# Performance work log

Measured on AMD Instinct MI355X. Metric: run time of the kernel, lower is better.

The kernel has to match this reference:

```python
import jax, jax.numpy as jnp
import numpy as np

B, N, K = 64, 1024, 20
HEADS, DIM_K, DIM_V, CH_RAISE = 8, 32, 32, 64
C_CAT = 4 * 2 + DIM_V  # 44


def setup_inputs() -> dict:
    key = jax.random.key(0)
    ks = jax.random.split(key, 16)

    def w(k, shape):
        fan_in = shape[-1]
        return jax.random.normal(k, shape, dtype=jnp.float32) / np.sqrt(fan_in)

    def gamma(k, n):
        return 1.0 + 0.1 * jax.random.normal(k, (n,), dtype=jnp.float32)

    def beta(k, n):
        return 0.1 * jax.random.normal(k, (n,), dtype=jnp.float32)

    return {
        "x": jax.random.normal(ks[0], (B, N, 4), dtype=jnp.float32),
        "W_h": w(ks[1], (DIM_V, 4)),              # mlp_h: conv2d 4 -> dim_v, 1x1
        "W1": w(ks[2], (CH_RAISE, C_CAT)),        # mlp conv2d 44 -> 64
        "g1": gamma(ks[3], CH_RAISE), "b1": beta(ks[4], CH_RAISE),
        "W2": w(ks[5], (CH_RAISE, CH_RAISE)),     # mlp conv2d 64 -> 64
        "g2": gamma(ks[6], CH_RAISE), "b2": beta(ks[7], CH_RAISE),
        "W_v": w(ks[8], (DIM_V, C_CAT)),          # mlp_v conv1d 44 -> 32
        "gv": gamma(ks[9], DIM_V), "bv": beta(ks[10], DIM_V),
        "W_k": w(ks[11], (DIM_K, C_CAT)),         # mlp_k conv1d 44 -> 32
        "W_q": w(ks[12], (HEADS * DIM_K, CH_RAISE)),  # mlp_q conv1d 64 -> 256
        "gq": gamma(ks[13], HEADS * DIM_K), "bq": beta(ks[14], HEADS * DIM_K),
    }


def _forward(x, W_h, W1, g1, b1, W2, g2, b2, W_v, gv, bv, W_k, W_q, gq, bq):
    xyz = x[..., :4]                 # [B,N,4]
    feat = xyz                       # use_norm=False -> feature = xyz
    b, n, _ = xyz.shape

    # squared pairwise distances [B,N,N]
    sq = jnp.sum(xyz * xyz, axis=-1)
    dist = -2.0 * jnp.einsum('bnc,bmc->bnm', xyz, xyz) + sq[:, :, None] + sq[:, None, :]

    # KNN: K smallest distances
    _, knn_idx = jax.lax.top_k(-dist, K)          # [B,N,K]
    bidx = jnp.arange(b)[:, None, None]
    neighbor_xyz = xyz[bidx, knn_idx]             # [B,N,K,4]
    grouped = feat[bidx, knn_idx]                 # [B,N,K,4]

    feat_t = jnp.transpose(feat, (0, 2, 1))       # [B,4,N]
    grouped_c = jnp.transpose(grouped, (0, 3, 1, 2))          # [B,4,N,K]
    gnorm = grouped_c - feat_t[..., None]                     # [B,4,N,K]
    rel = jnp.transpose(neighbor_xyz - xyz[:, :, None, :], (0, 3, 1, 2))  # [B,4,N,K]

    pos = jnp.einsum('vc,bcnk->bvnk', W_h, rel)               # [B,32,N,K]
    center = jnp.broadcast_to(feat_t[..., None], (b, 4, n, K))
    feature = jnp.concatenate([gnorm, center, pos], axis=1)   # [B,44,N,K]

    # mlp: two 1x1 conv + BN(eval, affine) + ReLU
    h = jnp.einsum('oc,bcnk->bonk', W1, feature)
    h = jax.nn.relu(g1[None, :, None, None] * h + b1[None, :, None, None])
    h = jnp.einsum('oc,bcnk->bonk', W2, h)
    h = jax.nn.relu(g2[None, :, None, None] * h + b2[None, :, None, None])
    feature_q = jnp.max(h, axis=-1)                           # [B,64,N]

    q = jnp.einsum('oc,bcn->bon', W_q, feature_q)             # [B,256,N]
    q = jax.nn.relu(gq[None, :, None] * q + bq[None, :, None])
    q = q.reshape(b, HEADS, DIM_K, n)                         # [B,h,d,N]

    v = jnp.einsum('vc,bcnk->bvnk', W_v, feature)             # [B,32,N,K]
    v = gv[None, :, None, None] * v + bv[None, :, None, None]
    v = jnp.transpose(v, (0, 2, 1, 3))                        # [B,N,v,K]

    kk = jnp.einsum('dc,bcnk->bdnk', W_k, feature)            # [B,32,N,K]
    kk = jax.nn.softmax(kk, axis=-1)
    kk = jnp.transpose(kk, (0, 2, 1, 3))                      # [B,N,d,K]

    kv = jnp.einsum('bndk,bnvk->bdvn', kk, v)                 # [B,d,v,N]
    out = jnp.einsum('bhdn,bdvn->bhvn', q, kv)                # [B,h,v,N]
    out = out.reshape(b, HEADS * DIM_V, n)                    # [B,256,N]
    return xyz, out


def reference(x, W_h, W1, g1, b1, W2, g2, b2, W_v, gv, bv, W_k, W_q, gq, bq):
    return _forward(x, W_h, W1, g1, b1, W2, g2, b2, W_v, gv, bv, W_k, W_q, gq, bq)
```

## Files before the change

### kernel.cpp

```cpp
#include <hip/hip_runtime.h>
#include <math.h>

#define NPTS 1024
#define KNBR 20
#define CH 64


typedef __attribute__((ext_vector_type(8))) short s16x8;
typedef __attribute__((ext_vector_type(4))) float f32x4;

static __device__ __forceinline__ ushort f2bf(float f) {
  uint u = __float_as_uint(f);
  uint r = (u + 0x7FFFu + ((u >> 16) & 1u)) >> 16;
  return (ushort)r;
}

static __device__ __forceinline__ uint pkbf(float a, float b) {
  uint ua = __float_as_uint(a) + 0x8000u;
  uint ub = __float_as_uint(b) + 0x8000u;
  return __builtin_amdgcn_perm(ub, ua, 0x07060302);
}

static __device__ __forceinline__ int mbcnt64(unsigned long long m) {
  return __builtin_amdgcn_mbcnt_hi((uint)(m >> 32),
                                   __builtin_amdgcn_mbcnt_lo((uint)m, 0));
}

__global__ __launch_bounds__(256) void k_prep(
    const float* __restrict__ Wh, const float* __restrict__ W1,
    const float* __restrict__ g1, const float* __restrict__ b1,
    const float* __restrict__ Wv, const float* __restrict__ Wk,
    const float* __restrict__ W2, const float* __restrict__ Wq,
    float* __restrict__ wp, ushort* __restrict__ w2b,
    ushort* __restrict__ wqb, ushort* __restrict__ w1b) {
  int t = threadIdx.x;
  {
    int o = t >> 2, c = t & 3;
    float acc = W1[o * 40 + c];
    #pragma unroll
    for (int v = 0; v < 32; ++v) acc = fmaf(W1[o * 40 + 8 + v], Wh[v * 4 + c], acc);
    float g = g1[o];
    wp[t] = g * acc;
    wp[256 + t] = g * W1[o * 40 + 4 + c];
  }
  if (t < 128) {
    int d = t >> 2, c = t & 3;
    float av = Wv[d * 40 + c];
    float ak = Wk[d * 40 + c];
    #pragma unroll
    for (int u = 0; u < 32; ++u) {
      av = fmaf(Wv[d * 40 + 8 + u], Wh[u * 4 + c], av);
      ak = fmaf(Wk[d * 40 + 8 + u], Wh[u * 4 + c], ak);
    }
    wp[512 + t] = av;
    wp[640 + t] = Wv[d * 40 + 4 + c];
    wp[768 + t] = ak;
    wp[896 + t] = Wk[d * 40 + 4 + c];
  }
  #pragma unroll
  for (int i = 0; i < 16; ++i) w2b[t * 16 + i] = f2bf(W2[t * 16 + i]);
  for (int i = 0; i < 64; ++i) wqb[t * 64 + i] = f2bf(Wq[t * 64 + i]);
  __syncthreads();
  for (int idx = t; idx < 2048; idx += 256) {
    int ch = idx >> 5, kk = idx & 31;
    float v = 0.f;
    if (kk < 4) v = wp[ch * 4 + kk];
    else if (kk < 8) v = wp[256 + ch * 4 + (kk - 4)];
    else if (kk == 8) v = b1[ch];
    w1b[idx] = f2bf(v);
  }
}

__global__ __launch_bounds__(256) void k_knn(const float4* __restrict__ xv,
                                             ushort* __restrict__ knn,
                                             float4* __restrict__ outx) {
  __shared__ float4 sx[NPTS];
  __shared__ float ssq[NPTS];
  __shared__ uint s_sk[4][64];
  __shared__ ushort s_sj[4][64];

  int t = threadIdx.x;
  int b = blockIdx.x >> 6, grp = blockIdx.x & 63;
  for (int j = t; j < NPTS; j += 256) {
    float4 p = xv[b * NPTS + j];
    sx[j] = p;
    ssq[j] = p.x * p.x + p.y * p.y + p.z * p.z + p.w * p.w;
    if (grp == 0) outx[b * NPTS + j] = p;
  }
  __syncthreads();

  int w = t >> 6, l = t & 63;

  #pragma unroll 1
  for (int i = 0; i < 4; ++i) {
    int cloc = grp * 16 + w * 4 + i;
    int gid20 = (b * NPTS + cloc) * KNBR;
    float4 c = sx[cloc];
    uint u[16];
    uint mn = 0xFFFFFFFFu;
    #pragma unroll
    for (int s = 0; s < 16; ++s) {
      int j = s * 64 + l;
      float4 q = sx[j];
      float dot = c.x * q.x;
      dot = fmaf(c.y, q.y, dot);
      dot = fmaf(c.z, q.z, dot);
      dot = fmaf(c.w, q.w, dot);
      float key = fmaf(-2.f, dot, ssq[j]);
      uint uu = __float_as_uint(key);
      uu = ((int)uu < 0) ? ~uu : (uu | 0x80000000u);
      u[s] = uu;
      mn = min(mn, uu);
    }

    uint T0 = 0;
    #pragma unroll
    for (int bit = 31; bit >= 0; --bit) {
      uint cand = T0 | (1u << bit);
      if (__popcll(__ballot(mn < cand)) < 20) T0 = cand;
    }

    int scnt = 0;
    #pragma unroll
    for (int s = 0; s < 16; ++s) scnt += (int)__popcll(__ballot(u[s] <= T0));

    if (scnt <= 64) {
      int base = 0;
      #pragma unroll
      for (int s = 0; s < 16; ++s) {
        unsigned long long mask = __ballot(u[s] <= T0);
        if (u[s] <= T0) {
          int off = base + mbcnt64(mask);
          s_sk[w][off] = u[s];
          s_sj[w][off] = (ushort)(s * 64 + l);
        }
        base += (int)__popcll(mask);
      }
      asm volatile("s_waitcnt lgkmcnt(0)" ::: "memory");
      __builtin_amdgcn_sched_barrier(0);
      uint uk = (l < scnt) ? s_sk[w][l] : 0xFFFFFFFFu;
      uint uj = (l < scnt) ? (uint)s_sj[w][l] : 0xFFFFu;

      uint u20 = 0;
      #pragma unroll
      for (int bit = 31; bit >= 0; --bit) {
        uint cand = u20 | (1u << bit);
        if (__popcll(__ballot(uk < cand)) < 20) u20 = cand;
      }
      int m = (int)__popcll(__ballot(uk < u20));
      int r = 20 - m;
      uint jr = 0;
      #pragma unroll
      for (int bit = 10; bit >= 0; --bit) {
        uint cand = jr | (1u << bit);
        if (__popcll(__ballot((uk == u20) && (uj < cand))) < r) jr = cand;
      }
      bool sel = (uk < u20) || ((uk == u20) && (uj <= jr));
      unsigned long long smask = __ballot(sel);
      int off = mbcnt64(smask);
      if (sel) knn[gid20 + off] = (ushort)uj;
    } else {
      uint u20 = 0;
      #pragma unroll 1
      for (int bit = 31; bit >= 0; --bit) {
        uint cand = u20 | (1u << bit);
        int cnt = 0;
        #pragma unroll
        for (int s = 0; s < 16; ++s)
          cnt += (int)__popcll(__ballot(u[s] < cand));
        if (cnt < 20) u20 = cand;
      }
      int base = 0;
      #pragma unroll
      for (int s = 0; s < 16; ++s) {
        unsigned long long mask = __ballot(u[s] < u20);
        if (u[s] < u20) knn[gid20 + base + mbcnt64(mask)] = (ushort)(s * 64 + l);
        base += (int)__popcll(mask);
      }
      int r = 20 - base;
      #pragma unroll
      for (int s = 0; s < 16; ++s) {
        unsigned long long mask = __ballot(u[s] == u20);
        int pos = mbcnt64(mask);
        int cntm = (int)__popcll(mask);
        int take = (r < cntm) ? r : cntm;
        if ((u[s] == u20) && (pos < take))
          knn[gid20 + base + pos] = (ushort)(s * 64 + l);
        base += take;
        r -= take;
      }
    }
  }
}

__global__ __launch_bounds__(256) void k_fused(
    const float4* __restrict__ xv, const ushort* __restrict__ knn,
    const float* __restrict__ wp, const ushort* __restrict__ w1b,
    const ushort* __restrict__ w2b, const ushort* __restrict__ wqb,
    const float* __restrict__ g2, const float* __restrict__ b2,
    const float* __restrict__ gq, const float* __restrict__ bq,
    const float* __restrict__ gv, const float* __restrict__ bv,
    float* __restrict__ o1) {
  __shared__ __align__(16) char smem[51200];
  char* s_h1 = smem;
  ushort* s_qb = (ushort*)smem;
  ushort* s_eb = (ushort*)(smem + 10496);
  float* s_out = (float*)(smem + 10496);
  float4* s_rel = (float4*)(smem + 40960);
  char* s_fqb = smem + 46080;
  float4* s_ctr = (float4*)(smem + 48384);
  ushort* s_ab = (ushort*)(smem + 40960);

  int t = threadIdx.x;
  int gid0 = blockIdx.x * 16;
  int bbase = (gid0 >> 10) << 10;
  int b = gid0 >> 10;
  int n0 = gid0 & 1023;
  int w = t >> 6, l = t & 63;
  int g = l >> 4, lane16 = l & 15;

  if (t < 16) s_ctr[t] = xv[gid0 + t];
  #pragma unroll
  for (int it2 = 0; it2 < 2; ++it2) {
    int idx = t + it2 * 256;
    if (idx < 320) {
      int p = (int)(((uint)idx * 3277u) >> 16);
      int k = idx - p * 20;
      int nb = (int)knn[(size_t)(gid0 + p) * KNBR + k];
      float4 nx = xv[bbase + nb];
      float4 ct = xv[gid0 + p];
      s_rel[p * 20 + k] =
          make_float4(nx.x - ct.x, nx.y - ct.y, nx.z - ct.z, nx.w - ct.w);
    }
  }
  __syncthreads();

  {
    s16x8 ah[4];
    #pragma unroll
    for (int m = 0; m < 4; ++m)
      ah[m] = *(const s16x8*)(w1b + (m * 16 + lane16) * 32 + g * 8);
    s16x8 bz = {0, 0, 0, 0, 0, 0, 0, 0};
    s16x8 bone = bz;
    bone[0] = (short)0x3F80;
    #pragma unroll
    for (int q = 0; q < 5; ++q) {
      int col = w * 80 + q * 16 + lane16;
      s16x8 bf;
      if (g == 0) {
        float4 r = s_rel[lane16 * 20 + 5 * w + q];
        float4 ct = s_ctr[lane16];
        union { uint4 u; s16x8 s; } cv;
        cv.u.x = pkbf(r.x, r.y);
        cv.u.y = pkbf(r.z, r.w);
        cv.u.z = pkbf(ct.x, ct.y);
        cv.u.w = pkbf(ct.z, ct.w);
        bf = cv.s;
      } else {
        bf = (g == 1) ? bone : bz;
      }
      int swz = (col & 7) << 4;
      #pragma unroll
      for (int m = 0; m < 4; ++m) {
        f32x4 acc = {0.f, 0.f, 0.f, 0.f};
        acc = __builtin_amdgcn_mfma_f32_16x16x32_bf16(ah[m], bf, acc, 0, 0, 0);
        uint2 hv;
        hv.x = pkbf(fmaxf(acc[0], 0.f), fmaxf(acc[1], 0.f));
        hv.y = pkbf(fmaxf(acc[2], 0.f), fmaxf(acc[3], 0.f));
        int byteoff = col * 128 + (m * 16 + g * 4) * 2;
        *(uint2*)(s_h1 + (byteoff ^ swz)) = hv;
      }
    }
  }
  __syncthreads();

  {
    int row0 = w * 16 + g * 4;
    s16x8 af0 = *(const s16x8*)(w2b + (w * 16 + lane16) * 64 + g * 8);
    s16x8 af1 = *(const s16x8*)(w2b + (w * 16 + lane16) * 64 + 32 + g * 8);
    float4 g2v = *(const float4*)(g2 + row0);
    float4 b2v = *(const float4*)(b2 + row0);
    float mx0 = 0.f, mx1 = 0.f, mx2 = 0.f, mx3 = 0.f;
    #pragma unroll 4
    for (int kt = 0; kt < 20; ++kt) {
      int col = kt * 16 + lane16;
      int rowbyte = col * 128;
      int swz = (col & 7) << 4;
      s16x8 bf0 = *(const s16x8*)(s_h1 + ((rowbyte + g * 16) ^ swz));
      s16x8 bf1 = *(const s16x8*)(s_h1 + ((rowbyte + 64 + g * 16) ^ swz));
      f32x4 acc = {0.f, 0.f, 0.f, 0.f};
      acc = __builtin_amdgcn_mfma_f32_16x16x32_bf16(af0, bf0, acc, 0, 0, 0);
      acc = __builtin_amdgcn_mfma_f32_16x16x32_bf16(af1, bf1, acc, 0, 0, 0);
      mx0 = fmaxf(mx0, fmaxf(fmaf(g2v.x, acc[0], b2v.x), 0.f));
      mx1 = fmaxf(mx1, fmaxf(fmaf(g2v.y, acc[1], b2v.y), 0.f));
      mx2 = fmaxf(mx2, fmaxf(fmaf(g2v.z, acc[2], b2v.z), 0.f));
      mx3 = fmaxf(mx3, fmaxf(fmaf(g2v.w, acc[3], b2v.w), 0.f));
    }
    uint2 u2;
    u2.x = pkbf(mx0, mx1);
    u2.y = pkbf(mx2, mx3);
    *(uint2*)(s_fqb + lane16 * 144 + row0 * 2) = u2;
  }
  __syncthreads();

  {
    s16x8 af[4][2];
    #pragma unroll
    for (int mm = 0; mm < 4; ++mm) {
      int row = w * 64 + mm * 16 + lane16;
      af[mm][0] = *(const s16x8*)(wqb + row * 64 + g * 8);
      af[mm][1] = *(const s16x8*)(wqb + row * 64 + 32 + g * 8);
    }
    s16x8 bf0 = *(const s16x8*)(s_fqb + lane16 * 144 + 0 * 64 + g * 16);
    s16x8 bf1 = *(const s16x8*)(s_fqb + lane16 * 144 + 1 * 64 + g * 16);
    #pragma unroll
    for (int mm = 0; mm < 4; ++mm) {
      f32x4 acc = {0.f, 0.f, 0.f, 0.f};
      acc = __builtin_amdgcn_mfma_f32_16x16x32_bf16(af[mm][0], bf0, acc, 0, 0, 0);
      acc = __builtin_amdgcn_mfma_f32_16x16x32_bf16(af[mm][1], bf1, acc, 0, 0, 0);
      int rbase = w * 64 + mm * 16 + g * 4;
      int h = rbase >> 5, d0 = rbase & 31;
      float4 gqv = *(const float4*)(gq + rbase);
      float4 bqv = *(const float4*)(bq + rbase);
      float v0 = fmaxf(fmaf(gqv.x, acc[0], bqv.x), 0.f);
      float v1 = fmaxf(fmaf(gqv.y, acc[1], bqv.y), 0.f);
      float v2 = fmaxf(fmaf(gqv.z, acc[2], bqv.z), 0.f);
      float v3 = fmaxf(fmaf(gqv.w, acc[3], bqv.w), 0.f);
      uint2 u2;
      u2.x = pkbf(v0, v1);
      u2.y = pkbf(v2, v3);
      *(uint2*)(s_qb + lane16 * 328 + h * 40 + d0) = u2;
    }
  }

  uint vp[2][10];
  {
    int d = t & 31, phalf = t >> 5;
    float4 wr = *(const float4*)(wp + 512 + 256 + d * 4);
    float4 wc = *(const float4*)(wp + 512 + 384 + d * 4);
    float4 vr_ = *(const float4*)(wp + 512 + 0 + d * 4);
    float4 vc_ = *(const float4*)(wp + 512 + 128 + d * 4);
    float gvd = gv[d], bvd = bv[d];
    #pragma unroll
    for (int i = 0; i < 2; ++i) {
      int p = phalf + 8 * i;
      float4 ct = s_ctr[p];
      float cb = fmaf(wc.x, ct.x, fmaf(wc.y, ct.y, fmaf(wc.z, ct.z, wc.w * ct.w)));
      float ev[KNBR];
      float sum = 0.f;
      #pragma unroll
      for (int k = 0; k < KNBR; ++k) {
        float4 r = s_rel[p * 20 + k];
        float kkv =
            fmaf(wr.x, r.x, fmaf(wr.y, r.y, fmaf(wr.z, r.z, fmaf(wr.w, r.w, cb))));
        ev[k] = __expf(kkv);
        sum += ev[k];
      }
      float cbv = fmaf(vc_.x, ct.x, fmaf(vc_.y, ct.y, fmaf(vc_.z, ct.z, vc_.w * ct.w)));
      float vv[KNBR];
      #pragma unroll
      for (int k = 0; k < KNBR; ++k) {
        float4 r = s_rel[p * 20 + k];
        float raw =
            fmaf(vr_.x, r.x, fmaf(vr_.y, r.y, fmaf(vr_.z, r.z, fmaf(vr_.w, r.w, cbv))));
        vv[k] = fmaf(gvd, raw, bvd);
      }
      float rs = 1.0f / sum;
      #pragma unroll
      for (int k = 0; k < KNBR; ++k)
        s_eb[(p * 20 + k) * 40 + d] = f2bf(ev[k] * rs);
      #pragma unroll
      for (int k2 = 0; k2 < 10; ++k2) vp[i][k2] = pkbf(vv[k2 * 2], vv[k2 * 2 + 1]);
    }
  }
  __syncthreads();

  #pragma unroll
  for (int pi2 = 0; pi2 < 4; ++pi2) {
    int plo = pi2 & 1, ii = pi2 >> 1;
    int pi = 2 * w + plo + 8 * ii;
    s16x8 qa = *(const s16x8*)(s_qb + pi * 328 + (lane16 & 7) * 40 + g * 8);
    #pragma unroll
    for (int tile = 0; tile < 2; ++tile) {
      int k = tile * 16 + lane16;
      int kc = (k < KNBR) ? k : (KNBR - 1);
      s16x8 eb = *(const s16x8*)(s_eb + (pi * 20 + kc) * 40 + g * 8);
      f32x4 acc = {0.f, 0.f, 0.f, 0.f};
      acc = __builtin_amdgcn_mfma_f32_16x16x32_bf16(qa, eb, acc, 0, 0, 0);
      if (g < 2) {
        if (k < KNBR) {
          #pragma unroll
          for (int r = 0; r < 4; ++r)
            s_ab[pi * 320 + (g * 4 + r) * 40 + k] = f2bf(acc[r]);
        } else {
          #pragma unroll
          for (int r = 0; r < 4; ++r) s_ab[pi * 320 + (g * 4 + r) * 40 + k] = 0;
        }
      }
    }
  }
  __syncthreads();

  #pragma unroll
  for (int pi2 = 0; pi2 < 4; ++pi2) {
    int plo = pi2 & 1, ii = pi2 >> 1;
    int pi = 2 * w + plo + 8 * ii;
    s16x8 aa = *(const s16x8*)(s_ab + pi * 320 + (lane16 & 7) * 40 + g * 8);
    #pragma unroll
    for (int vt = 0; vt < 2; ++vt) {
      int srcl4 = ((plo * 32 + vt * 16 + lane16) << 2);
      uint bu[4];
      #pragma unroll
      for (int i = 0; i < 4; ++i) {
        uint t0 = (uint)__builtin_amdgcn_ds_bpermute(srcl4, (int)vp[ii][i]);
        uint t1 = (uint)__builtin_amdgcn_ds_bpermute(srcl4, (int)vp[ii][4 + i]);
        uint t2 = (i < 2)
                      ? (uint)__builtin_amdgcn_ds_bpermute(srcl4, (int)vp[ii][8 + i])
                      : 0u;
        bu[i] = (g == 0) ? t0 : (g == 1) ? t1 : (g == 2) ? t2 : 0u;
      }
      union { uint4 u; s16x8 s; } bb;
      bb.u.x = bu[0]; bb.u.y = bu[1]; bb.u.z = bu[2]; bb.u.w = bu[3];
      f32x4 acc = {0.f, 0.f, 0.f, 0.f};
      acc = __builtin_amdgcn_mfma_f32_16x16x32_bf16(aa, bb.s, acc, 0, 0, 0);
      if (g < 2) {
        int v = vt * 16 + lane16;
        #pragma unroll
        for (int r = 0; r < 4; ++r) {
          int h = g * 4 + r;
          s_out[(h * 32 + v) * 17 + pi] = acc[r];
        }
      }
    }
  }
  __syncthreads();

  #pragma unroll
  for (int e = 0; e < 16; ++e) {
    int idx = t + e * 256;
    int hv = idx >> 4, pp = idx & 15;
    o1[b * 262144 + hv * 1024 + n0 + pp] = s_out[hv * 17 + pp];
  }
}

extern "C" void kernel_launch(void* const* d_in, const int* in_sizes, int n_in,
                              void* d_out, int out_size, void* d_ws, size_t ws_size,
                              hipStream_t stream) {
  const float* x = (const float*)d_in[0];
  const float* Wh = (const float*)d_in[1];
  const float* W1 = (const float*)d_in[2];
  const float* g1 = (const float*)d_in[3];
  const float* b1 = (const float*)d_in[4];
  const float* W2 = (const float*)d_in[5];
  const float* g2 = (const float*)d_in[6];
  const float* b2 = (const float*)d_in[7];
  const float* Wv = (const float*)d_in[8];
  const float* gv = (const float*)d_in[9];
  const float* bv = (const float*)d_in[10];
  const float* Wk = (const float*)d_in[11];
  const float* Wq = (const float*)d_in[12];
  const float* gq = (const float*)d_in[13];
  const float* bq = (const float*)d_in[14];
  float* out = (float*)d_out;

  ushort* knn = (ushort*)d_ws;
  float* wp = (float*)((char*)d_ws + 19398656);
  ushort* w2b = (ushort*)((char*)d_ws + 19402752);
  ushort* wqb = (ushort*)((char*)d_ws + 19410944);
  ushort* w1b = (ushort*)((char*)d_ws + 19443712);

  hipLaunchKernelGGL(k_prep, dim3(1), dim3(256), 0, stream, Wh, W1, g1, b1, Wv, Wk,
                     W2, Wq, wp, w2b, wqb, w1b);
  hipLaunchKernelGGL(k_knn, dim3(4096), dim3(256), 0, stream, (const float4*)x, knn,
                     (float4*)out);
  hipLaunchKernelGGL(k_fused, dim3(4096), dim3(256), 0, stream, (const float4*)x,
                     knn, wp, w1b, w2b, wqb, g2, b2, gq, bq, gv, bv, out + 262144);
}
```

Measured before the change: 161.5 us.

## Replace ballot radix selects in KNN with wave bitonic sorts and prefix scan

The KNN top-20 selection used 32-step ballot/popcount radix searches to find thresholds and a second pair of radix searches to break ties among the candidates. These are replaced by a 64-lane bitonic sort over the per-lane minima to get the threshold, a shuffle-based prefix scan for compaction offsets, and a 64-bit (key,index) bitonic sort of the compacted candidates that writes the first 20 directly. This cuts the serial ballot chain but adds many cross-lane shuffles, including 64-bit shuffles split into two 32-bit shuffles. The output order of the selected neighbours becomes sorted by distance instead of by index.

```diff
diff --git a/kernel.cpp b/kernel.cpp
--- a/kernel.cpp
+++ b/kernel.cpp
@@ -24,6 +24,13 @@
 static __device__ __forceinline__ int mbcnt64(unsigned long long m) {
   return __builtin_amdgcn_mbcnt_hi((uint)(m >> 32),
                                    __builtin_amdgcn_mbcnt_lo((uint)m, 0));
+}
+
+static __device__ __forceinline__ unsigned long long shflx64(
+    unsigned long long v, int m) {
+  uint lo = __shfl_xor((uint)v, m);
+  uint hi = __shfl_xor((uint)(v >> 32), m);
+  return (((unsigned long long)hi) << 32) | lo;
 }
 
 __global__ __launch_bounds__(256) void k_prep(
@@ -113,62 +120,71 @@
       mn = min(mn, uu);
     }
 
-    uint T0 = 0;
-    #pragma unroll
-    for (int bit = 31; bit >= 0; --bit) {
-      uint cand = T0 | (1u << bit);
-      if (__popcll(__ballot(mn < cand)) < 20) T0 = cand;
-    }
-
-    int scnt = 0;
-    #pragma unroll
-    for (int s = 0; s < 16; ++s) scnt += (int)__popcll(__ballot(u[s] <= T0));
+    uint sv = mn;
+    #pragma unroll
+    for (int kk2 = 2; kk2 <= 64; kk2 <<= 1) {
+      #pragma unroll
+      for (int j2 = kk2 >> 1; j2 > 0; j2 >>= 1) {
+        uint ov = __shfl_xor(sv, j2);
+        bool up = ((l & kk2) == 0);
+        bool keepmin = (((l & j2) == 0) == up);
+        uint lo_ = min(sv, ov), hi_ = max(sv, ov);
+        sv = keepmin ? lo_ : hi_;
+      }
+    }
+    uint T0 = __shfl(sv, 19);
+
+    int cnt = 0;
+    #pragma unroll
+    for (int s = 0; s < 16; ++s) cnt += (u[s] <= T0) ? 1 : 0;
+    int pfx = cnt;
+    #pragma unroll
+    for (int d2 = 1; d2 < 64; d2 <<= 1) {
+      int o = __shfl_up(pfx, d2);
+      if (l >= d2) pfx += o;
+    }
+    int scnt = __shfl(pfx, 63);
+    pfx -= cnt;
 
     if (scnt <= 64) {
-      int base = 0;
+      int off = pfx;
       #pragma unroll
       for (int s = 0; s < 16; ++s) {
-        unsigned long long mask = __ballot(u[s] <= T0);
         if (u[s] <= T0) {
-          int off = base + mbcnt64(mask);
           s_sk[w][off] = u[s];
           s_sj[w][off] = (ushort)(s * 64 + l);
+          ++off;
         }
-        base += (int)__popcll(mask);
       }
       asm volatile("s_waitcnt lgkmcnt(0)" ::: "memory");
       __builtin_amdgcn_sched_barrier(0);
       uint uk = (l < scnt) ? s_sk[w][l] : 0xFFFFFFFFu;
       uint uj = (l < scnt) ? (uint)s_sj[w][l] : 0xFFFFu;
-
-      uint u20 = 0;
-      #pragma unroll
-      for (int bit = 31; bit >= 0; --bit) {
-        uint cand = u20 | (1u << bit);
-        if (__popcll(__ballot(uk < cand)) < 20) u20 = cand;
-      }
-      int m = (int)__popcll(__ballot(uk < u20));
-      int r = 20 - m;
-      uint jr = 0;
-      #pragma unroll
-      for (int bit = 10; bit >= 0; --bit) {
-        uint cand = jr | (1u << bit);
-        if (__popcll(__ballot((uk == u20) && (uj < cand))) < r) jr = cand;
-      }
-      bool sel = (uk < u20) || ((uk == u20) && (uj <= jr));
-      unsigned long long smask = __ballot(sel);
-      int off = mbcnt64(smask);
-      if (sel) knn[gid20 + off] = (ushort)uj;
+      unsigned long long pv = (((unsigned long long)uk) << 16) | uj;
+
+      #pragma unroll
+      for (int kk2 = 2; kk2 <= 64; kk2 <<= 1) {
+        #pragma unroll
+        for (int j2 = kk2 >> 1; j2 > 0; j2 >>= 1) {
+          unsigned long long ov = shflx64(pv, j2);
+          bool up = ((l & kk2) == 0);
+          bool keepmin = (((l & j2) == 0) == up);
+          unsigned long long lo_ = (pv < ov) ? pv : ov;
+          unsigned long long hi_ = (pv < ov) ? ov : pv;
+          pv = keepmin ? lo_ : hi_;
+        }
+      }
+      if (l < KNBR) knn[gid20 + l] = (ushort)(pv & 0xFFFFu);
     } else {
       uint u20 = 0;
       #pragma unroll 1
       for (int bit = 31; bit >= 0; --bit) {
         uint cand = u20 | (1u << bit);
-        int cnt = 0;
+        int cnt2 = 0;
         #pragma unroll
         for (int s = 0; s < 16; ++s)
-          cnt += (int)__popcll(__ballot(u[s] < cand));
-        if (cnt < 20) u20 = cand;
+          cnt2 += (int)__popcll(__ballot(u[s] < cand));
+        if (cnt2 < 20) u20 = cand;
       }
       int base = 0;
       #pragma unroll
```

New measurement: 176.4 us. +9.3%, slower.

## Compute key and value projections with MFMA instead of scalar FMAs

Applied to the files above, without the earlier changes.

The prep kernel now packs the folded key and value weights, with the value scale and bias, into a bf16 matrix shaped like the first-layer weights. The fused kernel reuses the already-built B fragments to compute key logits and values with bf16 MFMAs into shared memory. It then reads them back per thread, replacing per-neighbor scalar dot products over the relative positions. This trades VALU work for extra MFMAs, two more barriers and shared-memory round trips, and key logits are now rounded to bf16 before the softmax exponent, which can affect accuracy.

```diff
diff --git a/kernel.cpp b/kernel.cpp
--- a/kernel.cpp
+++ b/kernel.cpp
@@ -29,10 +29,12 @@
 __global__ __launch_bounds__(256) void k_prep(
     const float* __restrict__ Wh, const float* __restrict__ W1,
     const float* __restrict__ g1, const float* __restrict__ b1,
-    const float* __restrict__ Wv, const float* __restrict__ Wk,
+    const float* __restrict__ Wv, const float* __restrict__ gv,
+    const float* __restrict__ bv, const float* __restrict__ Wk,
     const float* __restrict__ W2, const float* __restrict__ Wq,
     float* __restrict__ wp, ushort* __restrict__ w2b,
-    ushort* __restrict__ wqb, ushort* __restrict__ w1b) {
+    ushort* __restrict__ wqb, ushort* __restrict__ w1b,
+    ushort* __restrict__ wkvb) {
   int t = threadIdx.x;
   {
     int o = t >> 2, c = t & 3;
@@ -68,6 +70,21 @@
     else if (kk < 8) v = wp[256 + ch * 4 + (kk - 4)];
     else if (kk == 8) v = b1[ch];
     w1b[idx] = f2bf(v);
+  }
+  for (int idx = t; idx < 2048; idx += 256) {
+    int ch = idx >> 5, kk = idx & 31;
+    float v = 0.f;
+    if (ch < 32) {
+      if (kk < 4) v = wp[768 + ch * 4 + kk];
+      else if (kk < 8) v = wp[896 + ch * 4 + (kk - 4)];
+    } else {
+      int d = ch - 32;
+      float gvd = gv[d];
+      if (kk < 4) v = gvd * wp[512 + d * 4 + kk];
+      else if (kk < 8) v = gvd * wp[640 + d * 4 + (kk - 4)];
+      else if (kk == 8) v = bv[d];
+    }
+    wkvb[idx] = f2bf(v);
   }
 }
 
@@ -164,11 +181,11 @@
       #pragma unroll 1
       for (int bit = 31; bit >= 0; --bit) {
         uint cand = u20 | (1u << bit);
-        int cnt = 0;
+        int cnt2 = 0;
         #pragma unroll
         for (int s = 0; s < 16; ++s)
-          cnt += (int)__popcll(__ballot(u[s] < cand));
-        if (cnt < 20) u20 = cand;
+          cnt2 += (int)__popcll(__ballot(u[s] < cand));
+        if (cnt2 < 20) u20 = cand;
       }
       int base = 0;
       #pragma unroll
@@ -195,14 +212,14 @@
 
 __global__ __launch_bounds__(256) void k_fused(
     const float4* __restrict__ xv, const ushort* __restrict__ knn,
-    const float* __restrict__ wp, const ushort* __restrict__ w1b,
-    const ushort* __restrict__ w2b, const ushort* __restrict__ wqb,
+    const ushort* __restrict__ w1b, const ushort* __restrict__ w2b,
+    const ushort* __restrict__ wqb, const ushort* __restrict__ wkvb,
     const float* __restrict__ g2, const float* __restrict__ b2,
     const float* __restrict__ gq, const float* __restrict__ bq,
-    const float* __restrict__ gv, const float* __restrict__ bv,
     float* __restrict__ o1) {
   __shared__ __align__(16) char smem[51200];
   char* s_h1 = smem;
+  char* s_kv = smem;
   ushort* s_qb = (ushort*)smem;
   ushort* s_eb = (ushort*)(smem + 10496);
   float* s_out = (float*)(smem + 10496);
@@ -235,6 +252,7 @@
   }
   __syncthreads();
 
+  s16x8 bfv[5];
   {
     s16x8 ah[4];
     #pragma unroll
@@ -259,6 +277,7 @@
       } else {
         bf = (g == 1) ? bone : bz;
       }
+      bfv[q] = bf;
       int swz = (col & 7) << 4;
       #pragma unroll
       for (int m = 0; m < 4; ++m) {
@@ -304,6 +323,51 @@
   __syncthreads();
 
   {
+    s16x8 akv[4];
+    #pragma unroll
+    for (int m = 0; m < 4; ++m)
+      akv[m] = *(const s16x8*)(wkvb + (m * 16 + lane16) * 32 + g * 8);
+    #pragma unroll
+    for (int q = 0; q < 5; ++q) {
+      int col = w * 80 + q * 16 + lane16;
+      int swz = (col & 7) << 4;
+      #pragma unroll
+      for (int m = 0; m < 4; ++m) {
+        f32x4 acc = {0.f, 0.f, 0.f, 0.f};
+        acc = __builtin_amdgcn_mfma_f32_16x16x32_bf16(akv[m], bfv[q], acc, 0, 0, 0);
+        uint2 hv;
+        hv.x = pkbf(acc[0], acc[1]);
+        hv.y = pkbf(acc[2], acc[3]);
+        int byteoff = col * 128 + (m * 16 + g * 4) * 2;
+        *(uint2*)(s_kv + (byteoff ^ swz)) = hv;
+      }
+    }
+  }
+  __syncthreads();
+
+  uint kkpk[2][10], vp[2][10];
+  int dd = t & 31, phalf = t >> 5;
+  {
+    #pragma unroll
+    for (int i = 0; i < 2; ++i) {
+      int p = phalf + 8 * i;
+      int swz = (p & 7) << 4;
+      const char* kbase = s_kv + p * 128 + ((dd * 2) ^ swz);
+      const char* vbase = s_kv + p * 128 + (((64 + dd * 2)) ^ swz);
+      #pragma unroll
+      for (int k2 = 0; k2 < 10; ++k2) {
+        uint ka = *(const ushort*)(kbase + (2 * k2) * 2048);
+        uint kb = *(const ushort*)(kbase + (2 * k2 + 1) * 2048);
+        kkpk[i][k2] = ka | (kb << 16);
+        uint va = *(const ushort*)(vbase + (2 * k2) * 2048);
+        uint vb = *(const ushort*)(vbase + (2 * k2 + 1) * 2048);
+        vp[i][k2] = va | (vb << 16);
+      }
+    }
+  }
+  __syncthreads();
+
+  {
     s16x8 af[4][2];
     #pragma unroll
     for (int mm = 0; mm < 4; ++mm) {
@@ -332,45 +396,23 @@
       *(uint2*)(s_qb + lane16 * 328 + h * 40 + d0) = u2;
     }
   }
-
-  uint vp[2][10];
-  {
-    int d = t & 31, phalf = t >> 5;
-    float4 wr = *(const float4*)(wp + 512 + 256 + d * 4);
-    float4 wc = *(const float4*)(wp + 512 + 384 + d * 4);
-    float4 vr_ = *(const float4*)(wp + 512 + 0 + d * 4);
-    float4 vc_ = *(const float4*)(wp + 512 + 128 + d * 4);
-    float gvd = gv[d], bvd = bv[d];
+  {
     #pragma unroll
     for (int i = 0; i < 2; ++i) {
       int p = phalf + 8 * i;
-      float4 ct = s_ctr[p];
-      float cb = fmaf(wc.x, ct.x, fmaf(wc.y, ct.y, fmaf(wc.z, ct.z, wc.w * ct.w)));
       float ev[KNBR];
       float sum = 0.f;
       #pragma unroll
       for (int k = 0; k < KNBR; ++k) {
-        float4 r = s_rel[p * 20 + k];
-        float kkv =
-            fmaf(wr.x, r.x, fmaf(wr.y, r.y, fmaf(wr.z, r.z, fmaf(wr.w, r.w, cb))));
-        ev[k] = __expf(kkv);
+        uint bits = (k & 1) ? (kkpk[i][k >> 1] & 0xFFFF0000u)
+                            : (kkpk[i][k >> 1] << 16);
+        ev[k] = __expf(__uint_as_float(bits));
         sum += ev[k];
       }
-      float cbv = fmaf(vc_.x, ct.x, fmaf(vc_.y, ct.y, fmaf(vc_.z, ct.z, vc_.w * ct.w)));
-      float vv[KNBR];
-      #pragma unroll
-      for (int k = 0; k < KNBR; ++k) {
-        float4 r = s_rel[p * 20 + k];
-        float raw =
-            fmaf(vr_.x, r.x, fmaf(vr_.y, r.y, fmaf(vr_.z, r.z, fmaf(vr_.w, r.w, cbv))));
-        vv[k] = fmaf(gvd, raw, bvd);
-      }
       float rs = 1.0f / sum;
       #pragma unroll
       for (int k = 0; k < KNBR; ++k)
-        s_eb[(p * 20 + k) * 40 + d] = f2bf(ev[k] * rs);
-      #pragma unroll
-      for (int k2 = 0; k2 < 10; ++k2) vp[i][k2] = pkbf(vv[k2 * 2], vv[k2 * 2 + 1]);
+        s_eb[(p * 20 + k) * 40 + dd] = f2bf(ev[k] * rs);
     }
   }
   __syncthreads();
@@ -468,11 +510,12 @@
   ushort* w2b = (ushort*)((char*)d_ws + 19402752);
   ushort* wqb = (ushort*)((char*)d_ws + 19410944);
   ushort* w1b = (ushort*)((char*)d_ws + 19443712);
-
-  hipLaunchKernelGGL(k_prep, dim3(1), dim3(256), 0, stream, Wh, W1, g1, b1, Wv, Wk,
-                     W2, Wq, wp, w2b, wqb, w1b);
+  ushort* wkvb = (ushort*)((char*)d_ws + 19447808);
+
+  hipLaunchKernelGGL(k_prep, dim3(1), dim3(256), 0, stream, Wh, W1, g1, b1, Wv, gv,
+                     bv, Wk, W2, Wq, wp, w2b, wqb, w1b, wkvb);
   hipLaunchKernelGGL(k_knn, dim3(4096), dim3(256), 0, stream, (const float4*)x, knn,
                      (float4*)out);
   hipLaunchKernelGGL(k_fused, dim3(4096), dim3(256), 0, stream, (const float4*)x,
-                     knn, wp, w1b, w2b, wqb, g2, b2, gq, bq, gv, bv, out + 262144);
-}
+                     knn, w1b, w2b, wqb, wkvb, g2, b2, gq, bq, out + 262144);
+}
```

After: 172.1 us. 6.6% more time.

## Fuse KNN selection and feature MLP into one kernel via shared memory

Applied to the files above, without the earlier changes.

Merges the KNN kernel and the fused MLP/attention kernel into a single launch. Neighbor indices are kept in shared memory instead of going to global memory, and neighbor coordinates are gathered from the shared point cloud instead of global loads. This removes one launch, the round trip of the knn index buffer and the global gathers. In exchange the KNN-phase shared buffers are aliased into the larger fused-kernel region, which adds register and LDS pressure that may reduce occupancy.

```diff
diff --git a/kernel.cpp b/kernel.cpp
--- a/kernel.cpp
+++ b/kernel.cpp
@@ -71,30 +71,51 @@
   }
 }
 
-__global__ __launch_bounds__(256) void k_knn(const float4* __restrict__ xv,
-                                             ushort* __restrict__ knn,
-                                             float4* __restrict__ outx) {
-  __shared__ float4 sx[NPTS];
-  __shared__ float ssq[NPTS];
-  __shared__ uint s_sk[4][64];
-  __shared__ ushort s_sj[4][64];
+__global__ __launch_bounds__(256) void k_all(
+    const float4* __restrict__ xv, const float* __restrict__ wp,
+    const ushort* __restrict__ w1b, const ushort* __restrict__ w2b,
+    const ushort* __restrict__ wqb, const float* __restrict__ g2,
+    const float* __restrict__ b2, const float* __restrict__ gq,
+    const float* __restrict__ bq, const float* __restrict__ gv,
+    const float* __restrict__ bv, float4* __restrict__ outx,
+    float* __restrict__ o1) {
+  __shared__ __align__(16) char smem[51200];
+  float4* sx = (float4*)smem;
+  float* ssq = (float*)(smem + 16384);
+  char* s_h1 = smem;
+  ushort* s_qb = (ushort*)smem;
+  ushort* s_eb = (ushort*)(smem + 10496);
+  float* s_out = (float*)(smem + 10496);
+  float4* s_rel = (float4*)(smem + 40960);
+  char* s_fqb = smem + 46080;
+  float4* s_ctr = (float4*)(smem + 48384);
+  ushort* s_knn = (ushort*)(smem + 48640);
+  uint* s_sk = (uint*)(smem + 49280);
+  ushort* s_sj = (ushort*)(smem + 50304);
+  ushort* s_ab = (ushort*)(smem + 40960);
 
   int t = threadIdx.x;
-  int b = blockIdx.x >> 6, grp = blockIdx.x & 63;
+  int bid = blockIdx.x;
+  int b = bid >> 6, grp = bid & 63;
+  int gid0 = bid * 16;
+  int n0 = gid0 & 1023;
+  int w = t >> 6, l = t & 63;
+  int g = l >> 4, lane16 = l & 15;
+
   for (int j = t; j < NPTS; j += 256) {
     float4 p = xv[b * NPTS + j];
     sx[j] = p;
     ssq[j] = p.x * p.x + p.y * p.y + p.z * p.z + p.w * p.w;
     if (grp == 0) outx[b * NPTS + j] = p;
   }
-  __syncthreads();
-
-  int w = t >> 6, l = t & 63;
+  if (t < 16) s_ctr[t] = xv[gid0 + t];
+  __syncthreads();
 
   #pragma unroll 1
   for (int i = 0; i < 4; ++i) {
-    int cloc = grp * 16 + w * 4 + i;
-    int gid20 = (b * NPTS + cloc) * KNBR;
+    int lp = w * 4 + i;
+    int cloc = n0 + lp;
+    int lp20 = lp * KNBR;
     float4 c = sx[cloc];
     uint u[16];
     uint mn = 0xFFFFFFFFu;
@@ -131,15 +152,15 @@
         unsigned long long mask = __ballot(u[s] <= T0);
         if (u[s] <= T0) {
           int off = base + mbcnt64(mask);
-          s_sk[w][off] = u[s];
-          s_sj[w][off] = (ushort)(s * 64 + l);
+          s_sk[w * 64 + off] = u[s];
+          s_sj[w * 64 + off] = (ushort)(s * 64 + l);
         }
         base += (int)__popcll(mask);
       }
       asm volatile("s_waitcnt lgkmcnt(0)" ::: "memory");
       __builtin_amdgcn_sched_barrier(0);
-      uint uk = (l < scnt) ? s_sk[w][l] : 0xFFFFFFFFu;
-      uint uj = (l < scnt) ? (uint)s_sj[w][l] : 0xFFFFu;
+      uint uk = (l < scnt) ? s_sk[w * 64 + l] : 0xFFFFFFFFu;
+      uint uj = (l < scnt) ? (uint)s_sj[w * 64 + l] : 0xFFFFu;
 
       uint u20 = 0;
       #pragma unroll
@@ -158,23 +179,23 @@
       bool sel = (uk < u20) || ((uk == u20) && (uj <= jr));
       unsigned long long smask = __ballot(sel);
       int off = mbcnt64(smask);
-      if (sel) knn[gid20 + off] = (ushort)uj;
+      if (sel) s_knn[lp20 + off] = (ushort)uj;
     } else {
       uint u20 = 0;
       #pragma unroll 1
       for (int bit = 31; bit >= 0; --bit) {
         uint cand = u20 | (1u << bit);
-        int cnt = 0;
+        int cnt2 = 0;
         #pragma unroll
         for (int s = 0; s < 16; ++s)
-          cnt += (int)__popcll(__ballot(u[s] < cand));
-        if (cnt < 20) u20 = cand;
+          cnt2 += (int)__popcll(__ballot(u[s] < cand));
+        if (cnt2 < 20) u20 = cand;
       }
       int base = 0;
       #pragma unroll
       for (int s = 0; s < 16; ++s) {
         unsigned long long mask = __ballot(u[s] < u20);
-        if (u[s] < u20) knn[gid20 + base + mbcnt64(mask)] = (ushort)(s * 64 + l);
+        if (u[s] < u20) s_knn[lp20 + base + mbcnt64(mask)] = (ushort)(s * 64 + l);
         base += (int)__popcll(mask);
       }
       int r = 20 - base;
@@ -185,50 +206,23 @@
         int cntm = (int)__popcll(mask);
         int take = (r < cntm) ? r : cntm;
         if ((u[s] == u20) && (pos < take))
-          knn[gid20 + base + pos] = (ushort)(s * 64 + l);
+          s_knn[lp20 + base + pos] = (ushort)(s * 64 + l);
         base += take;
         r -= take;
       }
     }
   }
-}
-
-__global__ __launch_bounds__(256) void k_fused(
-    const float4* __restrict__ xv, const ushort* __restrict__ knn,
-    const float* __restrict__ wp, const ushort* __restrict__ w1b,
-    const ushort* __restrict__ w2b, const ushort* __restrict__ wqb,
-    const float* __restrict__ g2, const float* __restrict__ b2,
-    const float* __restrict__ gq, const float* __restrict__ bq,
-    const float* __restrict__ gv, const float* __restrict__ bv,
-    float* __restrict__ o1) {
-  __shared__ __align__(16) char smem[51200];
-  char* s_h1 = smem;
-  ushort* s_qb = (ushort*)smem;
-  ushort* s_eb = (ushort*)(smem + 10496);
-  float* s_out = (float*)(smem + 10496);
-  float4* s_rel = (float4*)(smem + 40960);
-  char* s_fqb = smem + 46080;
-  float4* s_ctr = (float4*)(smem + 48384);
-  ushort* s_ab = (ushort*)(smem + 40960);
-
-  int t = threadIdx.x;
-  int gid0 = blockIdx.x * 16;
-  int bbase = (gid0 >> 10) << 10;
-  int b = gid0 >> 10;
-  int n0 = gid0 & 1023;
-  int w = t >> 6, l = t & 63;
-  int g = l >> 4, lane16 = l & 15;
-
-  if (t < 16) s_ctr[t] = xv[gid0 + t];
+  __syncthreads();
+
   #pragma unroll
   for (int it2 = 0; it2 < 2; ++it2) {
     int idx = t + it2 * 256;
     if (idx < 320) {
       int p = (int)(((uint)idx * 3277u) >> 16);
       int k = idx - p * 20;
-      int nb = (int)knn[(size_t)(gid0 + p) * KNBR + k];
-      float4 nx = xv[bbase + nb];
-      float4 ct = xv[gid0 + p];
+      int nb = (int)s_knn[p * 20 + k];
+      float4 nx = sx[nb];
+      float4 ct = sx[n0 + p];
       s_rel[p * 20 + k] =
           make_float4(nx.x - ct.x, nx.y - ct.y, nx.z - ct.z, nx.w - ct.w);
     }
@@ -463,7 +457,6 @@
   const float* bq = (const float*)d_in[14];
   float* out = (float*)d_out;
 
-  ushort* knn = (ushort*)d_ws;
   float* wp = (float*)((char*)d_ws + 19398656);
   ushort* w2b = (ushort*)((char*)d_ws + 19402752);
   ushort* wqb = (ushort*)((char*)d_ws + 19410944);
@@ -471,8 +464,7 @@
 
   hipLaunchKernelGGL(k_prep, dim3(1), dim3(256), 0, stream, Wh, W1, g1, b1, Wv, Wk,
                      W2, Wq, wp, w2b, wqb, w1b);
-  hipLaunchKernelGGL(k_knn, dim3(4096), dim3(256), 0, stream, (const float4*)x, knn,
-                     (float4*)out);
-  hipLaunchKernelGGL(k_fused, dim3(4096), dim3(256), 0, stream, (const float4*)x,
-                     knn, wp, w1b, w2b, wqb, g2, b2, gq, bq, gv, bv, out + 262144);
-}
+  hipLaunchKernelGGL(k_all, dim3(4096), dim3(256), 0, stream, (const float4*)x, wp,
+                     w1b, w2b, wqb, g2, b2, gq, bq, gv, bv, (float4*)out,
+                     out + 262144);
+}
```

New measurement: 185.6 us. +14.9%, slower.
